# Optimization experiments

Hardware: AMD Instinct MI355X
Metric: run time of the kernel (lower is better)

Reference implementation:

```python
import jax, jax.numpy as jnp
import numpy as np

NHID = 256
B, T = 128, 2048


def setup_inputs() -> dict:
    key = jax.random.key(0)
    ks = jax.random.split(key, 7)
    s = 1.0 / np.sqrt(NHID)  # torch default uniform bound for RNN/Linear
    u = lambda k, shape, bound: jax.random.uniform(k, shape, jnp.float32, -bound, bound)
    return {
        "x": jax.random.normal(ks[0], (B, T, 1), jnp.float32),
        "W_ih": u(ks[1], (NHID, 1), s),
        "W_hh": u(ks[2], (NHID, NHID), s),
        "b_ih": u(ks[3], (NHID,), s),
        "b_hh": u(ks[4], (NHID,), s),
        "W_out": u(ks[5], (1, NHID), s),
        "b_out": u(ks[6], (1,), s),
    }


def reference(x, W_ih, W_hh, b_ih, b_hh, W_out, b_out):
    # x: [B, T, 1] -> time-major [T, B, 1]
    xt = jnp.transpose(x, (1, 0, 2))
    # Precompute input contribution for all steps: [T, B, H]
    xproj = xt @ W_ih.T + (b_ih + b_hh)

    def step(h, xp):  # h: [B, H], xp: [B, H]
        h_new = jnp.tanh(xp + h @ W_hh.T)
        return h_new, h_new

    h0 = jnp.zeros((x.shape[0], W_hh.shape[0]), dtype=x.dtype)
    _, ys = jax.lax.scan(step, h0, xproj)  # ys: [T, B, H]
    # Output projection then back to batch-major [B, T, 1]
    y = ys @ W_out.T + b_out
    return jnp.transpose(y, (1, 0, 2))
```

## Files before the change

### kernel.cpp

```cpp
#include <hip/hip_runtime.h>

#define HID  256
#define TT   2048
#define NB   128
#define NTHR 1024

template <int CTRL>
__device__ __forceinline__ float dpp_add(float v) {
    int t = __builtin_amdgcn_update_dpp(0, __float_as_int(v), CTRL, 0xF, 0xF, true);
    return v + __int_as_float(t);
}

__device__ __forceinline__ float tanh_fast(float x) {
    float e = __expf(2.0f * x);
    float r = __builtin_amdgcn_rcpf(e + 1.0f);
    return fmaf(-2.0f, r, 1.0f);
}


#define DECL_ROW(R) \
    float W##R##_0, W##R##_1, W##R##_2,  W##R##_3,  W##R##_4,  W##R##_5,  W##R##_6,  W##R##_7, \
          W##R##_8, W##R##_9, W##R##_10, W##R##_11, W##R##_12, W##R##_13, W##R##_14, W##R##_15;

#define LOAD_ROW(R) do { \
    const float4* wp_ = (const float4*)&W_hh[(4 * rg + R) * HID + 16 * c3]; \
    float4 a_ = wp_[0], b_ = wp_[1], c_ = wp_[2], d_ = wp_[3]; \
    W##R##_0  = a_.x; W##R##_1  = a_.y; W##R##_2  = a_.z; W##R##_3  = a_.w; \
    W##R##_4  = b_.x; W##R##_5  = b_.y; W##R##_6  = b_.z; W##R##_7  = b_.w; \
    W##R##_8  = c_.x; W##R##_9  = c_.y; W##R##_10 = c_.z; W##R##_11 = c_.w; \
    W##R##_12 = d_.x; W##R##_13 = d_.y; W##R##_14 = d_.z; W##R##_15 = d_.w; \
} while (0)

#define PIN_ROW(R) asm volatile("" \
    : "+v"(W##R##_0),  "+v"(W##R##_1),  "+v"(W##R##_2),  "+v"(W##R##_3), \
      "+v"(W##R##_4),  "+v"(W##R##_5),  "+v"(W##R##_6),  "+v"(W##R##_7), \
      "+v"(W##R##_8),  "+v"(W##R##_9),  "+v"(W##R##_10), "+v"(W##R##_11), \
      "+v"(W##R##_12), "+v"(W##R##_13), "+v"(W##R##_14), "+v"(W##R##_15))

#define FMA_ROW(R) do { \
    acc##R = fmaf(hx0,  W##R##_0,  acc##R); \
    acc##R = fmaf(hx1,  W##R##_1,  acc##R); \
    acc##R = fmaf(hx2,  W##R##_2,  acc##R); \
    acc##R = fmaf(hx3,  W##R##_3,  acc##R); \
    acc##R = fmaf(hx4,  W##R##_4,  acc##R); \
    acc##R = fmaf(hx5,  W##R##_5,  acc##R); \
    acc##R = fmaf(hx6,  W##R##_6,  acc##R); \
    acc##R = fmaf(hx7,  W##R##_7,  acc##R); \
    acc##R = fmaf(hx8,  W##R##_8,  acc##R); \
    acc##R = fmaf(hx9,  W##R##_9,  acc##R); \
    acc##R = fmaf(hx10, W##R##_10, acc##R); \
    acc##R = fmaf(hx11, W##R##_11, acc##R); \
    acc##R = fmaf(hx12, W##R##_12, acc##R); \
    acc##R = fmaf(hx13, W##R##_13, acc##R); \
    acc##R = fmaf(hx14, W##R##_14, acc##R); \
    acc##R = fmaf(hx15, W##R##_15, acc##R); \
} while (0)

#define RED16(A) do { \
    A = dpp_add<0xB1>(A); A = dpp_add<0x4E>(A); \
    A = dpp_add<0x124>(A); A = dpp_add<0x128>(A); \
} while (0)

__global__ __launch_bounds__(NTHR)
void rnn_persist(
    const float* __restrict__ x,
    const float* __restrict__ W_ih,
    const float* __restrict__ W_hh,
    const float* __restrict__ b_ih,
    const float* __restrict__ b_hh,
    const float* __restrict__ W_out,
    const float* __restrict__ b_out,
    float* __restrict__ y)
{
    __shared__ __align__(16) float s_h[2][8 * 36];
    __shared__ float s_x[TT];
    __shared__ float s_part[2][16];
    __shared__ float s_pad[22528];

    const int tid  = threadIdx.x;
    const int c3   = tid & 15;
    const int rg   = tid >> 4;
    const int lane = tid & 63;
    const int wv   = tid >> 6;
    const int b    = blockIdx.x;

    if (b == -1) {
        volatile float* vp = s_pad;
        vp[tid] = 1.0f;
        y[tid] = vp[tid];
    }

    for (int k = tid; k < TT; k += NTHR) s_x[k] = x[(size_t)b * TT + k];

    DECL_ROW(0) DECL_ROW(1) DECL_ROW(2) DECL_ROW(3)
    LOAD_ROW(0); LOAD_ROW(1); LOAD_ROW(2); LOAD_ROW(3);

    const int   myrow = 4 * rg + (c3 & 3);
    const float wih   = W_ih[myrow];
    const float bias  = b_ih[myrow] + b_hh[myrow];
    const float wo_my = W_out[myrow];
    const float bout  = b_out[0];

    if (tid < 256) {
        int wd = 36 * (tid >> 5) + (tid & 31);
        s_h[0][wd] = 0.0f;
        s_h[1][wd] = 0.0f;
    }
    __syncthreads();

    int p = 0;
    float* yrow = y + (size_t)b * TT;
    const int hwword = 36 * (myrow >> 5) + (myrow & 31);
    const int rdbase = 36 * (c3 >> 1) + 16 * (c3 & 1);

    for (int step = 0; step <= TT; ++step) {
        if (step >= 1 && wv == ((step - 1) & 15)) {
            float pp = s_part[(step - 1) & 1][lane & 15];
            pp = dpp_add<0xB1>(pp);
            pp = dpp_add<0x4E>(pp);
            pp = dpp_add<0x124>(pp);
            pp = dpp_add<0x128>(pp);
            if (lane == 0) yrow[step - 1] = pp + bout;
        }
        if (step == TT) break;

        PIN_ROW(0); PIN_ROW(1); PIN_ROW(2); PIN_ROW(3);

        const float xt = s_x[step];
        const float* hb = &s_h[p][rdbase];
        const float4 H0 = *(const float4*)(hb);
        const float4 H1 = *(const float4*)(hb + 4);
        const float4 H2 = *(const float4*)(hb + 8);
        const float4 H3 = *(const float4*)(hb + 12);
        const float hx0 = H0.x, hx1 = H0.y, hx2  = H0.z, hx3  = H0.w;
        const float hx4 = H1.x, hx5 = H1.y, hx6  = H1.z, hx7  = H1.w;
        const float hx8 = H2.x, hx9 = H2.y, hx10 = H2.z, hx11 = H2.w;
        const float hx12 = H3.x, hx13 = H3.y, hx14 = H3.z, hx15 = H3.w;

        float acc0 = 0.0f, acc1 = 0.0f, acc2 = 0.0f, acc3 = 0.0f;
        FMA_ROW(0); FMA_ROW(1); FMA_ROW(2); FMA_ROW(3);

        RED16(acc0); RED16(acc1); RED16(acc2); RED16(acc3);

        float s01 = (c3 & 1) ? acc1 : acc0;
        float s23 = (c3 & 1) ? acc3 : acc2;
        float dot = (c3 & 2) ? s23 : s01;
        float hn  = tanh_fast(fmaf(xt, wih, bias) + dot);

        if ((c3 & 12) == 0) s_h[p ^ 1][hwword] = hn;

        float pv = ((c3 & 12) == 0) ? hn * wo_my : 0.0f;
        pv = dpp_add<0xB1>(pv);
        pv = dpp_add<0x4E>(pv);
        pv = dpp_add<0x124>(pv);
        pv = dpp_add<0x128>(pv);
        pv = dpp_add<0x142>(pv);
        pv = dpp_add<0x143>(pv);
        if (lane == 63) s_part[step & 1][wv] = pv;

        __syncthreads();
        p ^= 1;
    }
}

extern "C" void kernel_launch(void* const* d_in, const int* in_sizes, int n_in,
                              void* d_out, int out_size, void* d_ws, size_t ws_size,
                              hipStream_t stream) {
    const float* x     = (const float*)d_in[0];
    const float* W_ih  = (const float*)d_in[1];
    const float* W_hh  = (const float*)d_in[2];
    const float* b_ih  = (const float*)d_in[3];
    const float* b_hh  = (const float*)d_in[4];
    const float* W_out = (const float*)d_in[5];
    const float* b_out = (const float*)d_in[6];
    float* y = (float*)d_out;

    hipLaunchKernelGGL(rnn_persist, dim3(NB), dim3(NTHR), 0, stream,
                       x, W_ih, W_hh, b_ih, b_hh, W_out, b_out, y);
}
```

Baseline: 1.483 ms.

## Pack W_hh to fp16 pairs and use v_fma_mix for recurrent dot

Adds a pre-pass kernel that converts W_hh to fp16 and packs pairs into a per-thread register layout in the workspace. The persistent RNN kernel then holds 32 packed registers per thread instead of 64 fp32 weights, and uses v_fma_mix_f32 to multiply fp16 weights by fp32 hidden values. This is meant to cut register pressure and possibly raise occupancy or scheduling freedom, at the cost of fp16 weight precision and an extra kernel launch. The FMA count per step stays the same.

```diff
diff --git a/kernel.cpp b/kernel.cpp
--- a/kernel.cpp
+++ b/kernel.cpp
@@ -17,44 +17,46 @@
     return fmaf(-2.0f, r, 1.0f);
 }
 
+__global__ void pack_w(const float* __restrict__ W, unsigned int* __restrict__ out) {
+    int j    = blockIdx.x * 256 + threadIdx.x;
+    int k    = j & 3;
+    int lane = (j >> 2) & 63;
+    int i    = (j >> 8) & 7;
+    int wv   = j >> 11;
+    int tid  = wv * 64 + lane;
+    int row  = 4 * (tid >> 4) + (i >> 1);
+    int col  = 16 * (tid & 15) + 8 * (i & 1) + 2 * k;
+    _Float16 lo = (_Float16)W[row * HID + col];
+    _Float16 hi = (_Float16)W[row * HID + col + 1];
+    unsigned short ulo, uhi;
+    __builtin_memcpy(&ulo, &lo, 2);
+    __builtin_memcpy(&uhi, &hi, 2);
+    out[j] = (unsigned int)ulo | ((unsigned int)uhi << 16);
+}
 
-#define DECL_ROW(R) \
-    float W##R##_0, W##R##_1, W##R##_2,  W##R##_3,  W##R##_4,  W##R##_5,  W##R##_6,  W##R##_7, \
-          W##R##_8, W##R##_9, W##R##_10, W##R##_11, W##R##_12, W##R##_13, W##R##_14, W##R##_15;
+#define MIXLO(ACC, W, H) asm("v_fma_mix_f32 %0, %1, %2, %0 op_sel_hi:[1,0,0]" \
+                             : "+v"(ACC) : "v"(W), "v"(H))
+#define MIXHI(ACC, W, H) asm("v_fma_mix_f32 %0, %1, %2, %0 op_sel:[1,0,0] op_sel_hi:[1,0,0]" \
+                             : "+v"(ACC) : "v"(W), "v"(H))
 
-#define LOAD_ROW(R) do { \
-    const float4* wp_ = (const float4*)&W_hh[(4 * rg + R) * HID + 16 * c3]; \
-    float4 a_ = wp_[0], b_ = wp_[1], c_ = wp_[2], d_ = wp_[3]; \
-    W##R##_0  = a_.x; W##R##_1  = a_.y; W##R##_2  = a_.z; W##R##_3  = a_.w; \
-    W##R##_4  = b_.x; W##R##_5  = b_.y; W##R##_6  = b_.z; W##R##_7  = b_.w; \
-    W##R##_8  = c_.x; W##R##_9  = c_.y; W##R##_10 = c_.z; W##R##_11 = c_.w; \
-    W##R##_12 = d_.x; W##R##_13 = d_.y; W##R##_14 = d_.z; W##R##_15 = d_.w; \
+#define DECL_CH(C) unsigned int Wc##C##_0, Wc##C##_1, Wc##C##_2, Wc##C##_3;
+#define LOAD_CH(C) do { \
+    uint4 t_ = wq[(wv * 8 + C) * 64 + lane]; \
+    Wc##C##_0 = t_.x; Wc##C##_1 = t_.y; Wc##C##_2 = t_.z; Wc##C##_3 = t_.w; \
 } while (0)
 
-#define PIN_ROW(R) asm volatile("" \
-    : "+v"(W##R##_0),  "+v"(W##R##_1),  "+v"(W##R##_2),  "+v"(W##R##_3), \
-      "+v"(W##R##_4),  "+v"(W##R##_5),  "+v"(W##R##_6),  "+v"(W##R##_7), \
-      "+v"(W##R##_8),  "+v"(W##R##_9),  "+v"(W##R##_10), "+v"(W##R##_11), \
-      "+v"(W##R##_12), "+v"(W##R##_13), "+v"(W##R##_14), "+v"(W##R##_15))
+#define FMA_CH(ACC, C, H0, H1, H2, H3, H4, H5, H6, H7) do { \
+    MIXLO(ACC, Wc##C##_0, H0); MIXHI(ACC, Wc##C##_0, H1); \
+    MIXLO(ACC, Wc##C##_1, H2); MIXHI(ACC, Wc##C##_1, H3); \
+    MIXLO(ACC, Wc##C##_2, H4); MIXHI(ACC, Wc##C##_2, H5); \
+    MIXLO(ACC, Wc##C##_3, H6); MIXHI(ACC, Wc##C##_3, H7); \
+} while (0)
 
-#define FMA_ROW(R) do { \
-    acc##R = fmaf(hx0,  W##R##_0,  acc##R); \
-    acc##R = fmaf(hx1,  W##R##_1,  acc##R); \
-    acc##R = fmaf(hx2,  W##R##_2,  acc##R); \
-    acc##R = fmaf(hx3,  W##R##_3,  acc##R); \
-    acc##R = fmaf(hx4,  W##R##_4,  acc##R); \
-    acc##R = fmaf(hx5,  W##R##_5,  acc##R); \
-    acc##R = fmaf(hx6,  W##R##_6,  acc##R); \
-    acc##R = fmaf(hx7,  W##R##_7,  acc##R); \
-    acc##R = fmaf(hx8,  W##R##_8,  acc##R); \
-    acc##R = fmaf(hx9,  W##R##_9,  acc##R); \
-    acc##R = fmaf(hx10, W##R##_10, acc##R); \
-    acc##R = fmaf(hx11, W##R##_11, acc##R); \
-    acc##R = fmaf(hx12, W##R##_12, acc##R); \
-    acc##R = fmaf(hx13, W##R##_13, acc##R); \
-    acc##R = fmaf(hx14, W##R##_14, acc##R); \
-    acc##R = fmaf(hx15, W##R##_15, acc##R); \
-} while (0)
+#define PIN16(A0,A1,A2,A3,A4,A5,A6,A7,A8,A9,Aa,Ab,Ac,Ad,Ae,Af) \
+    asm volatile("" : "+v"(A0), "+v"(A1), "+v"(A2), "+v"(A3), \
+                      "+v"(A4), "+v"(A5), "+v"(A6), "+v"(A7), \
+                      "+v"(A8), "+v"(A9), "+v"(Aa), "+v"(Ab), \
+                      "+v"(Ac), "+v"(Ad), "+v"(Ae), "+v"(Af))
 
 #define RED16(A) do { \
     A = dpp_add<0xB1>(A); A = dpp_add<0x4E>(A); \
@@ -65,7 +67,7 @@
 void rnn_persist(
     const float* __restrict__ x,
     const float* __restrict__ W_ih,
-    const float* __restrict__ W_hh,
+    const uint4* __restrict__ wq,
     const float* __restrict__ b_ih,
     const float* __restrict__ b_hh,
     const float* __restrict__ W_out,
@@ -92,8 +94,10 @@
 
     for (int k = tid; k < TT; k += NTHR) s_x[k] = x[(size_t)b * TT + k];
 
-    DECL_ROW(0) DECL_ROW(1) DECL_ROW(2) DECL_ROW(3)
-    LOAD_ROW(0); LOAD_ROW(1); LOAD_ROW(2); LOAD_ROW(3);
+    DECL_CH(0) DECL_CH(1) DECL_CH(2) DECL_CH(3)
+    DECL_CH(4) DECL_CH(5) DECL_CH(6) DECL_CH(7)
+    LOAD_CH(0); LOAD_CH(1); LOAD_CH(2); LOAD_CH(3);
+    LOAD_CH(4); LOAD_CH(5); LOAD_CH(6); LOAD_CH(7);
 
     const int   myrow = 4 * rg + (c3 & 3);
     const float wih   = W_ih[myrow];
@@ -124,7 +128,10 @@
         }
         if (step == TT) break;
 
-        PIN_ROW(0); PIN_ROW(1); PIN_ROW(2); PIN_ROW(3);
+        PIN16(Wc0_0, Wc0_1, Wc0_2, Wc0_3, Wc1_0, Wc1_1, Wc1_2, Wc1_3,
+              Wc2_0, Wc2_1, Wc2_2, Wc2_3, Wc3_0, Wc3_1, Wc3_2, Wc3_3);
+        PIN16(Wc4_0, Wc4_1, Wc4_2, Wc4_3, Wc5_0, Wc5_1, Wc5_2, Wc5_3,
+              Wc6_0, Wc6_1, Wc6_2, Wc6_3, Wc7_0, Wc7_1, Wc7_2, Wc7_3);
 
         const float xt = s_x[step];
         const float* hb = &s_h[p][rdbase];
@@ -138,7 +145,14 @@
         const float hx12 = H3.x, hx13 = H3.y, hx14 = H3.z, hx15 = H3.w;
 
         float acc0 = 0.0f, acc1 = 0.0f, acc2 = 0.0f, acc3 = 0.0f;
-        FMA_ROW(0); FMA_ROW(1); FMA_ROW(2); FMA_ROW(3);
+        FMA_CH(acc0, 0, hx0, hx1, hx2, hx3, hx4, hx5, hx6, hx7);
+        FMA_CH(acc0, 1, hx8, hx9, hx10, hx11, hx12, hx13, hx14, hx15);
+        FMA_CH(acc1, 2, hx0, hx1, hx2, hx3, hx4, hx5, hx6, hx7);
+        FMA_CH(acc1, 3, hx8, hx9, hx10, hx11, hx12, hx13, hx14, hx15);
+        FMA_CH(acc2, 4, hx0, hx1, hx2, hx3, hx4, hx5, hx6, hx7);
+        FMA_CH(acc2, 5, hx8, hx9, hx10, hx11, hx12, hx13, hx14, hx15);
+        FMA_CH(acc3, 6, hx0, hx1, hx2, hx3, hx4, hx5, hx6, hx7);
+        FMA_CH(acc3, 7, hx8, hx9, hx10, hx11, hx12, hx13, hx14, hx15);
 
         RED16(acc0); RED16(acc1); RED16(acc2); RED16(acc3);
 
@@ -174,7 +188,9 @@
     const float* W_out = (const float*)d_in[5];
     const float* b_out = (const float*)d_in[6];
     float* y = (float*)d_out;
+    unsigned int* wpk = (unsigned int*)d_ws;
 
+    hipLaunchKernelGGL(pack_w, dim3(128), dim3(256), 0, stream, W_hh, wpk);
     hipLaunchKernelGGL(rnn_persist, dim3(NB), dim3(NTHR), 0, stream,
-                       x, W_ih, W_hh, b_ih, b_hh, W_out, b_out, y);
+                       x, W_ih, (const uint4*)wpk, b_ih, b_hh, W_out, b_out, y);
 }
```

Result: slower. 1.995 ms (+34.5%).
